# Optimization experiments

Measured on AMD Instinct MI355X. Metric: run time of the kernel, lower is better.

Reference implementation:

```python
import jax, jax.numpy as jnp
import numpy as np

T, B, E, H = 2048, 2, 1024, 16

def setup_inputs() -> dict:
    rng = jax.random.key(0)
    ks = jax.random.split(rng, 7)
    s = 0.02
    return {
        "query": jax.random.normal(ks[0], (T, B, E), jnp.float32),
        "key": jax.random.normal(ks[1], (T, B, E), jnp.float32),
        "value": jax.random.normal(ks[2], (T, B, E), jnp.float32),
        "in_proj_weight": jax.random.normal(ks[3], (3 * E, E), jnp.float32) * s,
        "in_proj_bias": jax.random.normal(ks[4], (3 * E,), jnp.float32) * s,
        "out_proj_weight": jax.random.normal(ks[5], (E, E), jnp.float32) * s,
        "out_proj_bias": jax.random.normal(ks[6], (E,), jnp.float32) * s,
    }

def reference(query, key, value, in_proj_weight, in_proj_bias, out_proj_weight, out_proj_bias):
    tgt_len, bsz, embed_dim = query.shape
    num_heads = H
    head_dim = embed_dim // num_heads
    scaling = head_dim ** -0.5
    wq, wk, wv = jnp.split(in_proj_weight, 3, axis=0)
    bq, bk, bv = jnp.split(in_proj_bias, 3, axis=0)
    # projections: F.linear(x, W, b) = x @ W.T + b
    q = (query @ wq.T + bq) * scaling          # (T, B, E)
    k = key @ wk.T + bk                        # (S, B, E)
    v = value @ wv.T + bv                      # (S, B, E)
    # (len, B, E) -> (B*H, len, head_dim), matching torch view+transpose
    def to_heads(x):
        L = x.shape[0]
        return x.reshape(L, bsz * num_heads, head_dim).transpose(1, 0, 2)
    q, k, v = to_heads(q), to_heads(k), to_heads(v)
    scores = jnp.einsum('bqd,bkd->bqk', q, k)  # (B*H, T, S)
    attn = jax.nn.softmax(scores, axis=-1)
    out = jnp.einsum('bqk,bkd->bqd', attn, v)  # (B*H, T, head_dim)
    out = out.transpose(1, 0, 2).reshape(tgt_len, bsz, embed_dim)
    out = out @ out_proj_weight.T + out_proj_bias
    return out
```

## Files before the change

kernel.cpp:

```cpp
#include <hip/hip_runtime.h>
#include <cstdint>
#include <cstddef>

#define QSCALE 0.18033688011112042f

typedef __attribute__((ext_vector_type(8))) short bf16x8;
typedef __attribute__((ext_vector_type(4))) float f32x4;

#define MFMA(a, b, c) __builtin_amdgcn_mfma_f32_16x16x32_bf16(a, b, c, 0, 0, 0)

typedef union { unsigned int u[4]; bf16x8 b; } pku;

__device__ __forceinline__ unsigned short cvt_bf16(float x) {
  union { float f; unsigned int u; } v;
  v.f = x;
  unsigned int r = v.u + 0x7FFFu + ((v.u >> 16) & 1u);
  return (unsigned short)(r >> 16);
}

__device__ __forceinline__ void gll16(const void* g, void* l) {
  __builtin_amdgcn_global_load_lds(
      (const __attribute__((address_space(1))) unsigned int*)g,
      (__attribute__((address_space(3))) unsigned int*)l, 16, 0, 0);
}

__device__ __forceinline__ float fast_exp2(float x) {
#if __has_builtin(__builtin_amdgcn_exp2f)
  return __builtin_amdgcn_exp2f(x);
#else
  float r; asm("v_exp_f32 %0, %1" : "=v"(r) : "v"(x)); return r;
#endif
}

__device__ __forceinline__ unsigned int pack_bf16(float lo, float hi) {
  union { float f; unsigned int u; } a, b;
  a.f = lo; b.f = hi;
  return __builtin_amdgcn_perm(b.u + 0x8000u, a.u + 0x8000u, 0x07060302u);
}

__global__ void cvt_all(const float* __restrict__ q,
                        const float* __restrict__ k,
                        const float* __restrict__ v,
                        const float* __restrict__ ipw,
                        const float* __restrict__ opw,
                        unsigned short* __restrict__ dst) {
  const size_t i = ((size_t)blockIdx.x * 256 + threadIdx.x) * 8;
  const float* src;
  float scale = 1.0f;
  if (i < 4194304) src = q + i;
  else if (i < 8388608) src = k + (i - 4194304);
  else if (i < 12582912) src = v + (i - 8388608);
  else {
    const size_t w = i - 12582912;
    if (w < 3145728) { src = ipw + w; if (w < 1048576) scale = QSCALE; }
    else src = opw + (w - 3145728);
  }
  float4 a = *(const float4*)src;
  float4 b = *(const float4*)(src + 4);
  uint4 o;
  o.x = cvt_bf16(a.x * scale) | ((unsigned int)cvt_bf16(a.y * scale) << 16);
  o.y = cvt_bf16(a.z * scale) | ((unsigned int)cvt_bf16(a.w * scale) << 16);
  o.z = cvt_bf16(b.x * scale) | ((unsigned int)cvt_bf16(b.y * scale) << 16);
  o.w = cvt_bf16(b.z * scale) | ((unsigned int)cvt_bf16(b.w * scale) << 16);
  *(uint4*)(dst + i) = o;
}

__global__ __launch_bounds__(256, 3) void gemm_qkv(
    const unsigned short* __restrict__ X,
    const unsigned short* __restrict__ W,
    const float* __restrict__ bias,
    unsigned short* __restrict__ Qh,
    unsigned short* __restrict__ Kh,
    unsigned short* __restrict__ Vt)
{
  __shared__ unsigned short As[128 * 32];
  __shared__ unsigned short Bs[128 * 32];
  const int tid = threadIdx.x;
  const int wave = tid >> 6, lane = tid & 63;
  const int quad = lane >> 4, l16 = lane & 15;
  const int z = blockIdx.z;
  const int m0 = blockIdx.y * 128;
  const int n0 = blockIdx.x * 128;
  const unsigned short* Ab = X + (size_t)z * 4194304 + (size_t)m0 * 1024;
  const unsigned short* Bb = W + ((size_t)z * 1024 + n0) * 1024;
  const int wr = (wave >> 1) * 64, wc = (wave & 1) * 64;

  const f32x4 z4 = {0.f, 0.f, 0.f, 0.f};
  f32x4 acc[4][4];
#pragma unroll
  for (int i = 0; i < 4; ++i)
#pragma unroll
    for (int j = 0; j < 4; ++j) acc[i][j] = z4;

  const int c0 = wave * 128 + lane;
  for (int k0 = 0; k0 < 1024; k0 += 32) {
    __syncthreads();
#pragma unroll
    for (int j = 0; j < 2; ++j) {
      const int c = c0 + j * 64;
      const int row = c >> 2, kc = c & 3;
      gll16(Ab + (size_t)row * 1024 + k0 + kc * 8, &As[c * 8]);
      gll16(Bb + (size_t)row * 1024 + k0 + kc * 8, &Bs[c * 8]);
    }
    __syncthreads();
    bf16x8 af[4], bfr[4];
#pragma unroll
    for (int rt = 0; rt < 4; ++rt)
      af[rt] = *(const bf16x8*)&As[(wr + rt * 16 + l16) * 32 + quad * 8];
#pragma unroll
    for (int ct = 0; ct < 4; ++ct)
      bfr[ct] = *(const bf16x8*)&Bs[(wc + ct * 16 + l16) * 32 + quad * 8];
#pragma unroll
    for (int rt = 0; rt < 4; ++rt)
#pragma unroll
      for (int ct = 0; ct < 4; ++ct)
        acc[rt][ct] = MFMA(af[rt], bfr[ct], acc[rt][ct]);
  }

#pragma unroll
  for (int rt = 0; rt < 4; ++rt)
#pragma unroll
    for (int ct = 0; ct < 4; ++ct) {
      const int gn = n0 + wc + ct * 16 + l16;
      float bv = bias[z * 1024 + gn];
      if (z == 0) bv *= QSCALE;
      const int h = gn >> 6, d = gn & 63;
#pragma unroll
      for (int r = 0; r < 4; ++r) {
        const int gm = m0 + wr + rt * 16 + quad * 4 + r;
        const int t = gm >> 1, b = gm & 1;
        const int bh = b * 16 + h;
        const unsigned short o = cvt_bf16(acc[rt][ct][r] + bv);
        if (z == 0)      Qh[((size_t)bh * 2048 + t) * 64 + d] = o;
        else if (z == 1) Kh[((size_t)bh * 2048 + t) * 64 + d] = o;
        else {
          const int w32 = t & 31;
          const int tp = (t & ~31) | (((w32 >> 2) & 3) << 3) | ((w32 >> 4) << 2) | (w32 & 3);
          Vt[((size_t)bh * 64 + d) * 2048 + tp] = o;
        }
      }
    }
}

__global__ __launch_bounds__(256, 2) void attn(
    const unsigned short* __restrict__ Qh,
    const unsigned short* __restrict__ Kh,
    const unsigned short* __restrict__ Vt,
    unsigned short* __restrict__ O)
{
  __shared__ unsigned short Ks[128 * 64];
  __shared__ unsigned short Vs[64 * 128];
  const int tid = threadIdx.x;
  const int wave = tid >> 6, lane = tid & 63;
  const int quad = lane >> 4, l16 = lane & 15;
  const int qt = blockIdx.x, bh = blockIdx.y;
  const unsigned short* Qb = Qh + ((size_t)bh * 2048 + qt * 128 + wave * 32) * 64;
  const unsigned short* Kb = Kh + (size_t)bh * 2048 * 64;
  const unsigned short* Vb = Vt + (size_t)bh * 64 * 2048;

  bf16x8 qf[2][2];
#pragma unroll
  for (int rt = 0; rt < 2; ++rt)
#pragma unroll
    for (int kk = 0; kk < 2; ++kk)
      qf[rt][kk] = *(const bf16x8*)(Qb + (size_t)(rt * 16 + l16) * 64 + kk * 32 + quad * 8);

  const unsigned short* kp[4];
  const unsigned short* vp[4];
  unsigned short* kl[4];
  unsigned short* vl[4];
#pragma unroll
  for (int j = 0; j < 4; ++j) {
    const int c = wave * 256 + j * 64 + lane;
    const int r = c >> 3, cc = c & 7;
    kp[j] = Kb + (size_t)r * 64 + (cc ^ (r & 7)) * 8;
    kl[j] = &Ks[c * 8];
    const int r2 = c >> 4, cc2 = c & 15;
    vp[j] = Vb + (size_t)r2 * 2048 + (cc2 ^ (r2 & 15)) * 8;
    vl[j] = &Vs[c * 8];
  }

  pku ones;
  ones.u[0] = ones.u[1] = ones.u[2] = ones.u[3] = 0x3F803F80u;

  const f32x4 z4 = {0.f, 0.f, 0.f, 0.f};
  f32x4 oacc[2][4];
  f32x4 lacc[2] = {z4, z4};
#pragma unroll
  for (int rt = 0; rt < 2; ++rt)
#pragma unroll
    for (int c = 0; c < 4; ++c) oacc[rt][c] = z4;

#pragma unroll 1
  for (int it = 0; it < 16; ++it) {
    __syncthreads();
#pragma unroll
    for (int j = 0; j < 4; ++j) {
      gll16(kp[j], kl[j]);
      gll16(vp[j], vl[j]);
      kp[j] += 128 * 64;
      vp[j] += 128;
    }
    __syncthreads();

    unsigned int pkl_[2][8], pkh_[2][8];
#pragma unroll
    for (int ct = 0; ct < 8; ++ct) {
      f32x4 s0v = z4, s1v = z4;
#pragma unroll
      for (int kk = 0; kk < 2; ++kk) {
        const int R = ct * 16 + l16;
        const int phys = (kk * 4 + quad) ^ (R & 7);
        const bf16x8 kfr = *(const bf16x8*)&Ks[R * 64 + phys * 8];
        s0v = MFMA(kfr, qf[0][kk], s0v);
        s1v = MFMA(kfr, qf[1][kk], s1v);
      }
      f32x4 p0, p1;
#pragma unroll
      for (int r = 0; r < 4; ++r) { p0[r] = fast_exp2(s0v[r]); p1[r] = fast_exp2(s1v[r]); }
      pkl_[0][ct] = pack_bf16(p0[0], p0[1]);
      pkh_[0][ct] = pack_bf16(p0[2], p0[3]);
      pkl_[1][ct] = pack_bf16(p1[0], p1[1]);
      pkh_[1][ct] = pack_bf16(p1[2], p1[3]);
    }

#pragma unroll
    for (int kk2 = 0; kk2 < 4; ++kk2) {
      pku a0, a1;
      a0.u[0] = pkl_[0][kk2 * 2];     a0.u[1] = pkh_[0][kk2 * 2];
      a0.u[2] = pkl_[0][kk2 * 2 + 1]; a0.u[3] = pkh_[0][kk2 * 2 + 1];
      a1.u[0] = pkl_[1][kk2 * 2];     a1.u[1] = pkh_[1][kk2 * 2];
      a1.u[2] = pkl_[1][kk2 * 2 + 1]; a1.u[3] = pkh_[1][kk2 * 2 + 1];
#pragma unroll
      for (int ctd = 0; ctd < 4; ++ctd) {
        const int R = ctd * 16 + l16;
        const int phys = (kk2 * 4 + quad) ^ (R & 15);
        const bf16x8 vv = *(const bf16x8*)&Vs[R * 128 + phys * 8];
        oacc[0][ctd] = MFMA(a0.b, vv, oacc[0][ctd]);
        oacc[1][ctd] = MFMA(a1.b, vv, oacc[1][ctd]);
      }
      lacc[0] = MFMA(a0.b, ones.b, lacc[0]);
      lacc[1] = MFMA(a1.b, ones.b, lacc[1]);
    }
  }

  const int b = bh >> 4, h = bh & 15;
#pragma unroll
  for (int rt = 0; rt < 2; ++rt)
#pragma unroll
    for (int r = 0; r < 4; ++r) {
      const float inv = 1.0f / lacc[rt][r];
      const int t = qt * 128 + wave * 32 + rt * 16 + quad * 4 + r;
#pragma unroll
      for (int ctd = 0; ctd < 4; ++ctd) {
        const int col = h * 64 + ctd * 16 + l16;
        O[((size_t)t * 2 + b) * 1024 + col] = cvt_bf16(oacc[rt][ctd][r] * inv);
      }
    }
}

__global__ __launch_bounds__(256, 4) void gemm_out(
    const unsigned short* __restrict__ A,
    const unsigned short* __restrict__ W,
    const float* __restrict__ bias,
    float* __restrict__ out)
{
  __shared__ unsigned short As[128 * 32];
  __shared__ unsigned short Bs[64 * 32];
  const int tid = threadIdx.x;
  const int wave = tid >> 6, lane = tid & 63;
  const int quad = lane >> 4, l16 = lane & 15;
  const int m0 = blockIdx.y * 128;
  const int n0 = blockIdx.x * 64;
  const unsigned short* Ab = A + (size_t)m0 * 1024;
  const unsigned short* Bb = W + (size_t)n0 * 1024;
  const int wr = (wave >> 1) * 64, wc = (wave & 1) * 32;

  const f32x4 z4 = {0.f, 0.f, 0.f, 0.f};
  f32x4 acc[4][2];
#pragma unroll
  for (int i = 0; i < 4; ++i)
#pragma unroll
    for (int j = 0; j < 2; ++j) acc[i][j] = z4;

  for (int k0 = 0; k0 < 1024; k0 += 32) {
    __syncthreads();
#pragma unroll
    for (int j = 0; j < 3; ++j) {
      const int c = j * 256 + tid;
      if (j < 2) {
        const int row = c >> 2, kc = c & 3;
        gll16(Ab + (size_t)row * 1024 + k0 + kc * 8, &As[c * 8]);
      } else {
        const int bc = c - 512;
        const int row = bc >> 2, kc = bc & 3;
        gll16(Bb + (size_t)row * 1024 + k0 + kc * 8, &Bs[bc * 8]);
      }
    }
    __syncthreads();
    bf16x8 af[4], bfr[2];
#pragma unroll
    for (int rt = 0; rt < 4; ++rt)
      af[rt] = *(const bf16x8*)&As[(wr + rt * 16 + l16) * 32 + quad * 8];
#pragma unroll
    for (int ct = 0; ct < 2; ++ct)
      bfr[ct] = *(const bf16x8*)&Bs[(wc + ct * 16 + l16) * 32 + quad * 8];
#pragma unroll
    for (int rt = 0; rt < 4; ++rt)
#pragma unroll
      for (int ct = 0; ct < 2; ++ct)
        acc[rt][ct] = MFMA(af[rt], bfr[ct], acc[rt][ct]);
  }

#pragma unroll
  for (int rt = 0; rt < 4; ++rt)
#pragma unroll
    for (int ct = 0; ct < 2; ++ct) {
      const int gn = n0 + wc + ct * 16 + l16;
      const float bv = bias[gn];
#pragma unroll
      for (int r = 0; r < 4; ++r) {
        const int gm = m0 + wr + rt * 16 + quad * 4 + r;
        out[(size_t)gm * 1024 + gn] = acc[rt][ct][r] + bv;
      }
    }
}

extern "C" void kernel_launch(void* const* d_in, const int* in_sizes, int n_in,
                              void* d_out, int out_size, void* d_ws, size_t ws_size,
                              hipStream_t stream) {
  const float* q   = (const float*)d_in[0];
  const float* k   = (const float*)d_in[1];
  const float* v   = (const float*)d_in[2];
  const float* ipw = (const float*)d_in[3];
  const float* ipb = (const float*)d_in[4];
  const float* opw = (const float*)d_in[5];
  const float* opb = (const float*)d_in[6];

  unsigned short* ws = (unsigned short*)d_ws;
  unsigned short* X  = ws;
  unsigned short* Wb = ws + 12582912;
  unsigned short* Wo = ws + 15728640;
  unsigned short* Qh = ws + 16777216;
  unsigned short* Kh = ws + 20971520;
  unsigned short* Vx = ws + 25165824;
  unsigned short* Oa = ws + 29360128;

  cvt_all<<<dim3(8192), 256, 0, stream>>>(q, k, v, ipw, opw, ws);
  gemm_qkv<<<dim3(8, 32, 3), 256, 0, stream>>>(X, Wb, ipb, Qh, Kh, Vx);
  attn<<<dim3(16, 32), 256, 0, stream>>>(Qh, Kh, Vx, Oa);
  gemm_out<<<dim3(16, 32), 256, 0, stream>>>(Oa, Wo, opb, (float*)d_out);
}
```

Baseline: 216.3 us.

## Deepen GEMM K-tiles with XOR swizzle, remap blocks across XCDs, halve attention q-tile

Both GEMMs now stage 64-wide K tiles with an XOR-swizzled LDS layout, which halves the number of barrier pairs and aims to avoid LDS bank conflicts. All three kernels remap the flat block index so that consecutive blocks spread across the 8 XCDs and neighbouring tiles share L2. The attention kernel now handles 64 queries per block (16 per wave) with twice as many blocks and a launch bound of 4, trading less K/V reuse per block for more occupancy. The larger LDS tiles may reduce occupancy in the GEMMs.

```diff
diff --git a/kernel.cpp b/kernel.cpp
--- a/kernel.cpp
+++ b/kernel.cpp
@@ -73,14 +73,16 @@
     unsigned short* __restrict__ Kh,
     unsigned short* __restrict__ Vt)
 {
-  __shared__ unsigned short As[128 * 32];
-  __shared__ unsigned short Bs[128 * 32];
+  __shared__ unsigned short As[128 * 64];
+  __shared__ unsigned short Bs[128 * 64];
   const int tid = threadIdx.x;
   const int wave = tid >> 6, lane = tid & 63;
   const int quad = lane >> 4, l16 = lane & 15;
-  const int z = blockIdx.z;
-  const int m0 = blockIdx.y * 128;
-  const int n0 = blockIdx.x * 128;
+  const int flat = blockIdx.x + (blockIdx.y << 3) + (blockIdx.z << 8);
+  const int nf = (flat & 7) * 96 + (flat >> 3);
+  const int z = nf >> 8;
+  const int m0 = ((nf >> 3) & 31) * 128;
+  const int n0 = (nf & 7) * 128;
   const unsigned short* Ab = X + (size_t)z * 4194304 + (size_t)m0 * 1024;
   const unsigned short* Bb = W + ((size_t)z * 1024 + n0) * 1024;
   const int wr = (wave >> 1) * 64, wc = (wave & 1) * 64;
@@ -92,29 +94,36 @@
 #pragma unroll
     for (int j = 0; j < 4; ++j) acc[i][j] = z4;
 
-  const int c0 = wave * 128 + lane;
-  for (int k0 = 0; k0 < 1024; k0 += 32) {
-    __syncthreads();
-#pragma unroll
-    for (int j = 0; j < 2; ++j) {
-      const int c = c0 + j * 64;
-      const int row = c >> 2, kc = c & 3;
+  for (int k0 = 0; k0 < 1024; k0 += 64) {
+    __syncthreads();
+#pragma unroll
+    for (int j = 0; j < 4; ++j) {
+      const int c = j * 256 + tid;
+      const int row = c >> 3, pc = c & 7;
+      const int kc = pc ^ (row & 7);
       gll16(Ab + (size_t)row * 1024 + k0 + kc * 8, &As[c * 8]);
       gll16(Bb + (size_t)row * 1024 + k0 + kc * 8, &Bs[c * 8]);
     }
     __syncthreads();
-    bf16x8 af[4], bfr[4];
-#pragma unroll
-    for (int rt = 0; rt < 4; ++rt)
-      af[rt] = *(const bf16x8*)&As[(wr + rt * 16 + l16) * 32 + quad * 8];
-#pragma unroll
-    for (int ct = 0; ct < 4; ++ct)
-      bfr[ct] = *(const bf16x8*)&Bs[(wc + ct * 16 + l16) * 32 + quad * 8];
-#pragma unroll
-    for (int rt = 0; rt < 4; ++rt)
-#pragma unroll
-      for (int ct = 0; ct < 4; ++ct)
-        acc[rt][ct] = MFMA(af[rt], bfr[ct], acc[rt][ct]);
+#pragma unroll
+    for (int kk = 0; kk < 2; ++kk) {
+      bf16x8 af[4], bfr[4];
+#pragma unroll
+      for (int rt = 0; rt < 4; ++rt) {
+        const int row = wr + rt * 16 + l16;
+        af[rt] = *(const bf16x8*)&As[row * 64 + ((kk * 4 + quad) ^ (row & 7)) * 8];
+      }
+#pragma unroll
+      for (int ct = 0; ct < 4; ++ct) {
+        const int row = wc + ct * 16 + l16;
+        bfr[ct] = *(const bf16x8*)&Bs[row * 64 + ((kk * 4 + quad) ^ (row & 7)) * 8];
+      }
+#pragma unroll
+      for (int rt = 0; rt < 4; ++rt)
+#pragma unroll
+        for (int ct = 0; ct < 4; ++ct)
+          acc[rt][ct] = MFMA(af[rt], bfr[ct], acc[rt][ct]);
+    }
   }
 
 #pragma unroll
@@ -142,7 +151,7 @@
     }
 }
 
-__global__ __launch_bounds__(256, 2) void attn(
+__global__ __launch_bounds__(256, 4) void attn(
     const unsigned short* __restrict__ Qh,
     const unsigned short* __restrict__ Kh,
     const unsigned short* __restrict__ Vt,
@@ -153,17 +162,17 @@
   const int tid = threadIdx.x;
   const int wave = tid >> 6, lane = tid & 63;
   const int quad = lane >> 4, l16 = lane & 15;
-  const int qt = blockIdx.x, bh = blockIdx.y;
-  const unsigned short* Qb = Qh + ((size_t)bh * 2048 + qt * 128 + wave * 32) * 64;
+  const int flat = blockIdx.x + (blockIdx.y << 5);
+  const int nf = (flat & 7) * 128 + (flat >> 3);
+  const int qt = nf & 31, bh = nf >> 5;
+  const unsigned short* Qb = Qh + ((size_t)bh * 2048 + qt * 64 + wave * 16) * 64;
   const unsigned short* Kb = Kh + (size_t)bh * 2048 * 64;
   const unsigned short* Vb = Vt + (size_t)bh * 64 * 2048;
 
-  bf16x8 qf[2][2];
-#pragma unroll
-  for (int rt = 0; rt < 2; ++rt)
-#pragma unroll
-    for (int kk = 0; kk < 2; ++kk)
-      qf[rt][kk] = *(const bf16x8*)(Qb + (size_t)(rt * 16 + l16) * 64 + kk * 32 + quad * 8);
+  bf16x8 qf[2];
+#pragma unroll
+  for (int kk = 0; kk < 2; ++kk)
+    qf[kk] = *(const bf16x8*)(Qb + (size_t)l16 * 64 + kk * 32 + quad * 8);
 
   const unsigned short* kp[4];
   const unsigned short* vp[4];
@@ -184,12 +193,10 @@
   ones.u[0] = ones.u[1] = ones.u[2] = ones.u[3] = 0x3F803F80u;
 
   const f32x4 z4 = {0.f, 0.f, 0.f, 0.f};
-  f32x4 oacc[2][4];
-  f32x4 lacc[2] = {z4, z4};
-#pragma unroll
-  for (int rt = 0; rt < 2; ++rt)
-#pragma unroll
-    for (int c = 0; c < 4; ++c) oacc[rt][c] = z4;
+  f32x4 oacc[4];
+  f32x4 lacc = z4;
+#pragma unroll
+  for (int c = 0; c < 4; ++c) oacc[c] = z4;
 
 #pragma unroll 1
   for (int it = 0; it < 16; ++it) {
@@ -203,60 +210,51 @@
     }
     __syncthreads();
 
-    unsigned int pkl_[2][8], pkh_[2][8];
+    unsigned int pkl_[8], pkh_[8];
 #pragma unroll
     for (int ct = 0; ct < 8; ++ct) {
-      f32x4 s0v = z4, s1v = z4;
+      f32x4 sv = z4;
 #pragma unroll
       for (int kk = 0; kk < 2; ++kk) {
         const int R = ct * 16 + l16;
         const int phys = (kk * 4 + quad) ^ (R & 7);
         const bf16x8 kfr = *(const bf16x8*)&Ks[R * 64 + phys * 8];
-        s0v = MFMA(kfr, qf[0][kk], s0v);
-        s1v = MFMA(kfr, qf[1][kk], s1v);
-      }
-      f32x4 p0, p1;
-#pragma unroll
-      for (int r = 0; r < 4; ++r) { p0[r] = fast_exp2(s0v[r]); p1[r] = fast_exp2(s1v[r]); }
-      pkl_[0][ct] = pack_bf16(p0[0], p0[1]);
-      pkh_[0][ct] = pack_bf16(p0[2], p0[3]);
-      pkl_[1][ct] = pack_bf16(p1[0], p1[1]);
-      pkh_[1][ct] = pack_bf16(p1[2], p1[3]);
+        sv = MFMA(kfr, qf[kk], sv);
+      }
+      f32x4 p;
+#pragma unroll
+      for (int r = 0; r < 4; ++r) p[r] = fast_exp2(sv[r]);
+      pkl_[ct] = pack_bf16(p[0], p[1]);
+      pkh_[ct] = pack_bf16(p[2], p[3]);
     }
 
 #pragma unroll
     for (int kk2 = 0; kk2 < 4; ++kk2) {
-      pku a0, a1;
-      a0.u[0] = pkl_[0][kk2 * 2];     a0.u[1] = pkh_[0][kk2 * 2];
-      a0.u[2] = pkl_[0][kk2 * 2 + 1]; a0.u[3] = pkh_[0][kk2 * 2 + 1];
-      a1.u[0] = pkl_[1][kk2 * 2];     a1.u[1] = pkh_[1][kk2 * 2];
-      a1.u[2] = pkl_[1][kk2 * 2 + 1]; a1.u[3] = pkh_[1][kk2 * 2 + 1];
+      pku a0;
+      a0.u[0] = pkl_[kk2 * 2];     a0.u[1] = pkh_[kk2 * 2];
+      a0.u[2] = pkl_[kk2 * 2 + 1]; a0.u[3] = pkh_[kk2 * 2 + 1];
 #pragma unroll
       for (int ctd = 0; ctd < 4; ++ctd) {
         const int R = ctd * 16 + l16;
         const int phys = (kk2 * 4 + quad) ^ (R & 15);
         const bf16x8 vv = *(const bf16x8*)&Vs[R * 128 + phys * 8];
-        oacc[0][ctd] = MFMA(a0.b, vv, oacc[0][ctd]);
-        oacc[1][ctd] = MFMA(a1.b, vv, oacc[1][ctd]);
-      }
-      lacc[0] = MFMA(a0.b, ones.b, lacc[0]);
-      lacc[1] = MFMA(a1.b, ones.b, lacc[1]);
+        oacc[ctd] = MFMA(a0.b, vv, oacc[ctd]);
+      }
+      lacc = MFMA(a0.b, ones.b, lacc);
     }
   }
 
   const int b = bh >> 4, h = bh & 15;
 #pragma unroll
-  for (int rt = 0; rt < 2; ++rt)
-#pragma unroll
-    for (int r = 0; r < 4; ++r) {
-      const float inv = 1.0f / lacc[rt][r];
-      const int t = qt * 128 + wave * 32 + rt * 16 + quad * 4 + r;
-#pragma unroll
-      for (int ctd = 0; ctd < 4; ++ctd) {
-        const int col = h * 64 + ctd * 16 + l16;
-        O[((size_t)t * 2 + b) * 1024 + col] = cvt_bf16(oacc[rt][ctd][r] * inv);
-      }
-    }
+  for (int r = 0; r < 4; ++r) {
+    const float inv = 1.0f / lacc[r];
+    const int t = qt * 64 + wave * 16 + quad * 4 + r;
+#pragma unroll
+    for (int ctd = 0; ctd < 4; ++ctd) {
+      const int col = h * 64 + ctd * 16 + l16;
+      O[((size_t)t * 2 + b) * 1024 + col] = cvt_bf16(oacc[ctd][r] * inv);
+    }
+  }
 }
 
 __global__ __launch_bounds__(256, 4) void gemm_out(
@@ -265,13 +263,15 @@
     const float* __restrict__ bias,
     float* __restrict__ out)
 {
-  __shared__ unsigned short As[128 * 32];
-  __shared__ unsigned short Bs[64 * 32];
+  __shared__ unsigned short As[128 * 64];
+  __shared__ unsigned short Bs[64 * 64];
   const int tid = threadIdx.x;
   const int wave = tid >> 6, lane = tid & 63;
   const int quad = lane >> 4, l16 = lane & 15;
-  const int m0 = blockIdx.y * 128;
-  const int n0 = blockIdx.x * 64;
+  const int flat = blockIdx.x + (blockIdx.y << 4);
+  const int nf = (flat & 7) * 64 + (flat >> 3);
+  const int m0 = (nf >> 4) * 128;
+  const int n0 = (nf & 15) * 64;
   const unsigned short* Ab = A + (size_t)m0 * 1024;
   const unsigned short* Bb = W + (size_t)n0 * 1024;
   const int wr = (wave >> 1) * 64, wc = (wave & 1) * 32;
@@ -283,33 +283,42 @@
 #pragma unroll
     for (int j = 0; j < 2; ++j) acc[i][j] = z4;
 
-  for (int k0 = 0; k0 < 1024; k0 += 32) {
-    __syncthreads();
-#pragma unroll
-    for (int j = 0; j < 3; ++j) {
+  for (int k0 = 0; k0 < 1024; k0 += 64) {
+    __syncthreads();
+#pragma unroll
+    for (int j = 0; j < 4; ++j) {
       const int c = j * 256 + tid;
-      if (j < 2) {
-        const int row = c >> 2, kc = c & 3;
-        gll16(Ab + (size_t)row * 1024 + k0 + kc * 8, &As[c * 8]);
-      } else {
-        const int bc = c - 512;
-        const int row = bc >> 2, kc = bc & 3;
-        gll16(Bb + (size_t)row * 1024 + k0 + kc * 8, &Bs[bc * 8]);
-      }
-    }
-    __syncthreads();
-    bf16x8 af[4], bfr[2];
-#pragma unroll
-    for (int rt = 0; rt < 4; ++rt)
-      af[rt] = *(const bf16x8*)&As[(wr + rt * 16 + l16) * 32 + quad * 8];
-#pragma unroll
-    for (int ct = 0; ct < 2; ++ct)
-      bfr[ct] = *(const bf16x8*)&Bs[(wc + ct * 16 + l16) * 32 + quad * 8];
-#pragma unroll
-    for (int rt = 0; rt < 4; ++rt)
-#pragma unroll
-      for (int ct = 0; ct < 2; ++ct)
-        acc[rt][ct] = MFMA(af[rt], bfr[ct], acc[rt][ct]);
+      const int row = c >> 3, pc = c & 7;
+      const int kc = pc ^ (row & 7);
+      gll16(Ab + (size_t)row * 1024 + k0 + kc * 8, &As[c * 8]);
+    }
+#pragma unroll
+    for (int j = 0; j < 2; ++j) {
+      const int c = j * 256 + tid;
+      const int row = c >> 3, pc = c & 7;
+      const int kc = pc ^ (row & 7);
+      gll16(Bb + (size_t)row * 1024 + k0 + kc * 8, &Bs[c * 8]);
+    }
+    __syncthreads();
+#pragma unroll
+    for (int kk = 0; kk < 2; ++kk) {
+      bf16x8 af[4], bfr[2];
+#pragma unroll
+      for (int rt = 0; rt < 4; ++rt) {
+        const int row = wr + rt * 16 + l16;
+        af[rt] = *(const bf16x8*)&As[row * 64 + ((kk * 4 + quad) ^ (row & 7)) * 8];
+      }
+#pragma unroll
+      for (int ct = 0; ct < 2; ++ct) {
+        const int row = wc + ct * 16 + l16;
+        bfr[ct] = *(const bf16x8*)&Bs[row * 64 + ((kk * 4 + quad) ^ (row & 7)) * 8];
+      }
+#pragma unroll
+      for (int rt = 0; rt < 4; ++rt)
+#pragma unroll
+        for (int ct = 0; ct < 2; ++ct)
+          acc[rt][ct] = MFMA(af[rt], bfr[ct], acc[rt][ct]);
+    }
   }
 
 #pragma unroll
@@ -348,6 +357,6 @@
 
   cvt_all<<<dim3(8192), 256, 0, stream>>>(q, k, v, ipw, opw, ws);
   gemm_qkv<<<dim3(8, 32, 3), 256, 0, stream>>>(X, Wb, ipb, Qh, Kh, Vx);
-  attn<<<dim3(16, 32), 256, 0, stream>>>(Qh, Kh, Vx, Oa);
+  attn<<<dim3(32, 32), 256, 0, stream>>>(Qh, Kh, Vx, Oa);
   gemm_out<<<dim3(16, 32), 256, 0, stream>>>(Oa, Wo, opb, (float*)d_out);
 }
```

Result: no change. 215.0 us (-0.6%).
